# Optimization experiments

Measured on AMD Instinct MI355X. Metric: run time of the kernel, lower is better.

Reference implementation:

```python
import jax, jax.numpy as jnp
import numpy as np

D_MODEL = 1024
H = 16
D_K = D_MODEL // H
D_FF = 4096
EPS = 1e-6
NEG = -1e9


def setup_inputs() -> dict:
    key = jax.random.key(0)
    ks = jax.random.split(key, 8)
    B, S = 2, 2048
    src = jax.random.normal(ks[0], (B, S, D_MODEL), dtype=jnp.float32)
    src_mask = jnp.ones((B, 1, 1, S), dtype=jnp.int32)
    sc = 1.0 / np.sqrt(D_MODEL)
    wq = jax.random.normal(ks[1], (D_MODEL, D_MODEL), jnp.float32) * sc
    wk = jax.random.normal(ks[2], (D_MODEL, D_MODEL), jnp.float32) * sc
    wv = jax.random.normal(ks[3], (D_MODEL, D_MODEL), jnp.float32) * sc
    wo = jax.random.normal(ks[4], (D_MODEL, D_MODEL), jnp.float32) * sc
    w1 = jax.random.normal(ks[5], (D_FF, D_MODEL), jnp.float32) * sc
    b1 = jnp.zeros((D_FF,), jnp.float32)
    w2 = jax.random.normal(ks[6], (D_MODEL, D_FF), jnp.float32) * (1.0 / np.sqrt(D_FF))
    b2 = jnp.zeros((D_MODEL,), jnp.float32)
    a1 = jnp.ones((1,), jnp.float32)
    be1 = jnp.zeros((1,), jnp.float32)
    a2 = jnp.ones((1,), jnp.float32)
    be2 = jnp.zeros((1,), jnp.float32)
    return dict(src=src, src_mask=src_mask, wq=wq, wk=wk, wv=wv, wo=wo,
                w1=w1, b1=b1, w2=w2, b2=b2, a1=a1, be1=be1, a2=a2, be2=be2)


def layer_norm(x, alpha, bias):
    # torch: mean + unbiased std (ddof=1), eps added to std
    mean = jnp.mean(x, axis=-1, keepdims=True)
    std = jnp.sqrt(jnp.var(x, axis=-1, keepdims=True, ddof=1))
    return alpha * (x - mean) / (std + EPS) + bias


def mha(x, mask, wq, wk, wv, wo):
    B, S, _ = x.shape
    def split(t):  # [B,S,D] -> [B,H,S,D_K]
        return t.reshape(B, S, H, D_K).transpose(0, 2, 1, 3)
    q = split(x @ wq.T)
    k = split(x @ wk.T)
    v = split(x @ wv.T)
    scores = jnp.einsum('bhqd,bhkd->bhqk', q, k) / np.sqrt(D_K)
    scores = jnp.where(mask == 0, NEG, scores)
    attn = jax.nn.softmax(scores, axis=-1)
    out = jnp.einsum('bhqk,bhkd->bhqd', attn, v)
    out = out.transpose(0, 2, 1, 3).reshape(B, S, D_MODEL)
    return out @ wo.T


def reference(src, src_mask, wq, wk, wv, wo, w1, b1, w2, b2, a1, be1, a2, be2):
    x = layer_norm(src, a1, be1)
    src = src + mha(x, src_mask, wq, wk, wv, wo)
    x = layer_norm(src, a2, be2)
    ff = jax.nn.relu(x @ w1.T + b1) @ w2.T + b2
    return src + ff
```

## Files before the change

kernel.cpp:

```cpp
#include <hip/hip_runtime.h>
#include <hip/hip_bf16.h>

typedef unsigned short u16;
typedef unsigned int u32;
typedef float floatx4 __attribute__((ext_vector_type(4)));
typedef __bf16 bf16x8 __attribute__((ext_vector_type(8)));
typedef u16 ushort4v __attribute__((ext_vector_type(4)));
typedef u16 ushort8v __attribute__((ext_vector_type(8)));

#define DEVI static __device__ __forceinline__

DEVI u16 f2bf(float f) {
    u32 u = __builtin_bit_cast(u32, f);
    u += 0x7fffu + ((u >> 16) & 1u);
    return (u16)(u >> 16);
}
DEVI float bf2f(u16 h) { return __builtin_bit_cast(float, (u32)h << 16); }

DEVI float fexp2(float x) { return __builtin_amdgcn_exp2f(x); }

DEVI u32 cvtpk_bf16(float lo, float hi) {
    u32 r;
    asm("v_cvt_pk_bf16_f32 %0, %1, %2" : "=v"(r) : "v"(lo), "v"(hi));
    return r;
}

DEVI void async_cp16(const u16* g, u16* l) {
    __builtin_amdgcn_global_load_lds((const __attribute__((address_space(1))) u32*)g,
                                     (__attribute__((address_space(3))) u32*)l, 16, 0, 0);
}

template<int N> DEVI void wait_vmcnt() {
    if constexpr (N == 2)      asm volatile("s_waitcnt vmcnt(2)" ::: "memory");
    else if constexpr (N == 3) asm volatile("s_waitcnt vmcnt(3)" ::: "memory");
    else if constexpr (N == 4) asm volatile("s_waitcnt vmcnt(4)" ::: "memory");
    else if constexpr (N == 6) asm volatile("s_waitcnt vmcnt(6)" ::: "memory");
    else if constexpr (N == 8) asm volatile("s_waitcnt vmcnt(8)" ::: "memory");
    else static_assert(N == 2, "add vmcnt case");
}

template<int BM, int BN, int RW, int CW, bool QKV3, int NSPLIT, bool XSWZ,
         bool BIAS, bool RELU, bool RESID, bool OBF16, bool VTW>
__global__ __launch_bounds__(256) void gemm_nt(
    const u16* __restrict__ A,
    const u16* __restrict__ W0, const u16* __restrict__ W1, const u16* __restrict__ W2,
    const float* __restrict__ bias, const float* __restrict__ resid,
    void* __restrict__ o0, void* __restrict__ o1, void* __restrict__ o2,
    void* __restrict__ o3, int K, int lda, int Nper, int NX)
{
    static_assert(RW * CW == 4, "4 waves");
    constexpr int WM = BM / RW, WN = BN / CW;
    constexpr int MI = WM / 16, NI = WN / 16;
    constexpr int LPT = BM / 64 + BN / 64;
    __shared__ __align__(16) u16 As[3][BM * 32];
    __shared__ __align__(16) u16 Bs[3][BN * 32];
    const int tid = threadIdx.x;
    const int w = tid >> 6, lane = tid & 63;
    const int q = lane >> 4, ml = lane & 15;
    const int wr = w / CW, wc = w % CW;
    int bx = blockIdx.x, by = blockIdx.y;
    if (XSWZ) {
        const int gx = gridDim.x, gy = gridDim.y;
        int L = by * gx + bx;
        int xcd = L & 7, s = L >> 3;
        int mb = gy >> 3;
        by = xcd * mb + s % mb;
        bx = s / mb;
    }
    const int m0 = by * BM;
    size_t kbase = 0;
    const u16* W = W0;
    void* outp = o0;
    if (NSPLIT > 1) {
        int part = bx / NX; bx -= part * NX; kbase = (size_t)part * K;
        outp = (part == 0) ? o0 : (part == 1 ? o1 : (part == 2 ? o2 : o3));
    }
    int n0 = bx * BN;
    bool vwrite = false;
    if (QKV3) {
        int sel = n0 / Nper;
        n0 -= sel * Nper;
        W = (sel == 0) ? W0 : (sel == 1 ? W1 : W2);
        outp = (sel == 0) ? o0 : (sel == 1 ? o1 : o2);
        if (VTW) vwrite = (sel == 2);
    }

    auto stage = [&](int buf, int kt) {
#pragma unroll
        for (int p = 0; p < BM / 64; ++p) {
            int g = p * 256 + tid;
            int r = g >> 2, s = g & 3;
            int c = s ^ ((r >> 1) & 3);
            async_cp16(A + (size_t)(m0 + r) * lda + kbase + kt + c * 8,
                       &As[buf][(p * 256 + w * 64) * 8]);
        }
#pragma unroll
        for (int p = 0; p < BN / 64; ++p) {
            int g = p * 256 + tid;
            int r = g >> 2, s = g & 3;
            int c = s ^ ((r >> 1) & 3);
            async_cp16(W + (size_t)(n0 + r) * lda + kbase + kt + c * 8,
                       &Bs[buf][(p * 256 + w * 64) * 8]);
        }
    };

    const floatx4 fzero = {0.f, 0.f, 0.f, 0.f};
    floatx4 acc[MI][NI];
#pragma unroll
    for (int i = 0; i < MI; ++i)
#pragma unroll
        for (int j = 0; j < NI; ++j) acc[i][j] = fzero;

    const int nt = K >> 5;
    stage(0, 0);
    stage(1, 32);
    int cb = 0, nb = 2;
    for (int it = 0, kt = 0; it < nt; ++it, kt += 32) {
        wait_vmcnt<LPT>();
        __builtin_amdgcn_s_barrier();
        __builtin_amdgcn_sched_barrier(0);
        if (it + 2 < nt) stage(nb, kt + 64);
        __builtin_amdgcn_sched_barrier(0);
        const u16* Asb = As[cb];
        const u16* Bsb = Bs[cb];
        bf16x8 af[MI], bfr[NI];
#pragma unroll
        for (int i = 0; i < MI; ++i) {
            int rm = wr * WM + i * 16 + ml;
            int s = q ^ ((rm >> 1) & 3);
            af[i] = *(const bf16x8*)&Asb[(rm * 4 + s) * 8];
        }
#pragma unroll
        for (int j = 0; j < NI; ++j) {
            int rn = wc * WN + j * 16 + ml;
            int s = q ^ ((rn >> 1) & 3);
            bfr[j] = *(const bf16x8*)&Bsb[(rn * 4 + s) * 8];
        }
#pragma unroll
        for (int i = 0; i < MI; ++i)
#pragma unroll
            for (int j = 0; j < NI; ++j)
                acc[i][j] = __builtin_amdgcn_mfma_f32_16x16x32_bf16(af[i], bfr[j], acc[i][j], 0, 0, 0);
        cb = cb == 2 ? 0 : cb + 1;
        nb = nb == 2 ? 0 : nb + 1;
    }

#pragma unroll
    for (int j = 0; j < NI; ++j) {
        int gn = n0 + wc * WN + j * 16 + ml;
        float bj = 0.f;
        if (BIAS) bj = bias[gn];
#pragma unroll
        for (int i = 0; i < MI; ++i) {
            int gm0 = m0 + wr * WM + i * 16 + q * 4;
            if (VTW && vwrite) {
                int bb = gm0 >> 11, sres = gm0 & 2047;
                ushort4v o = {f2bf(acc[i][j][0]), f2bf(acc[i][j][1]),
                              f2bf(acc[i][j][2]), f2bf(acc[i][j][3])};
                *(ushort4v*)&((u16*)o3)[(size_t)(bb * 1024 + gn) * 2048 + sres] = o;
            } else {
#pragma unroll
                for (int r = 0; r < 4; ++r) {
                    size_t idx = (size_t)(gm0 + r) * Nper + gn;
                    float v = acc[i][j][r] + bj;
                    if (RELU) v = fmaxf(v, 0.f);
                    if (RESID) v += resid[idx];
                    if (OBF16) ((u16*)outp)[idx] = f2bf(v);
                    else       ((float*)outp)[idx] = v;
                }
            }
        }
    }
}

__global__ __launch_bounds__(256, 2) void flash9(
    const u16* __restrict__ Q, const u16* __restrict__ Kg,
    const u16* __restrict__ Vt, const float* __restrict__ biasv,
    u16* __restrict__ O)
{
    __shared__ __align__(16) u16 smem[24576];
    const int tid = threadIdx.x;
    const int w = tid >> 6, lane = tid & 63;
    const int qw = w & 1, kv = w >> 1;
    const int q = lane >> 4, ml = lane & 15;
    const int b = blockIdx.y >> 4, h = blockIdx.y & 15;
    const size_t rowQ = (size_t)(b * 2048 + blockIdx.x * 128);
    const float KSC = 0.125f * 1.4426950408889634f;
    const floatx4 fzero = {0.f, 0.f, 0.f, 0.f};

    bf16x8 qa[4][2];
#pragma unroll
    for (int qg = 0; qg < 4; ++qg)
#pragma unroll
        for (int c = 0; c < 2; ++c)
            qa[qg][c] = *(const bf16x8*)&Q[(rowQ + qw * 64 + qg * 16 + ml) * 1024
                                           + h * 64 + q * 8 + c * 32];

    auto stage = [&](int buf, int it) {
        {
            int row = tid >> 3, sl = tid & 7;
            int ch = sl ^ ((row & 3) | (((row >> 3) & 1) << 2));
#pragma unroll
            for (int hf = 0; hf < 2; ++hf)
                async_cp16(Kg + (size_t)(b * 2048 + hf * 1024 + it * 32 + row) * 1024
                               + h * 64 + ch * 8,
                           &smem[(hf * 3 + buf) * 2048 + w * 512]);
        }
        {
            int row = tid >> 2, sl = tid & 3;
            int ch = sl ^ ((row >> 1) & 3);
#pragma unroll
            for (int hf = 0; hf < 2; ++hf)
                async_cp16(Vt + (size_t)(b * 1024 + h * 64 + row) * 2048
                               + hf * 1024 + it * 32 + ch * 8,
                           &smem[12288 + (hf * 3 + buf) * 2048 + w * 512]);
        }
    };

    floatx4 oacc[4][4];
    float lsum[4] = {0.f, 0.f, 0.f, 0.f};
#pragma unroll
    for (int qg = 0; qg < 4; ++qg)
#pragma unroll
        for (int d = 0; d < 4; ++d) oacc[qg][d] = fzero;

    const int swk = (ml & 3) | (((ml >> 2) & 1) << 2);
    const int re = ((ml >> 2) << 3) + (ml & 3);

    stage(0, 0);
    stage(1, 1);
    int cb = 0, nb = 2;
    for (int it = 0; it < 32; ++it) {
        asm volatile("s_waitcnt vmcnt(4)" ::: "memory");
        __builtin_amdgcn_s_barrier();
        __builtin_amdgcn_sched_barrier(0);
        const int s0 = kv * 1024 + it * 32;
        const float4 be = *(const float4*)&biasv[b * 2048 + s0 + q * 8];
        const float4 bo = *(const float4*)&biasv[b * 2048 + s0 + q * 8 + 4];
        __builtin_amdgcn_sched_barrier(0);
        stage(nb, it + 2 < 32 ? it + 2 : 31);

        const u16* Kb = &smem[(kv * 3 + cb) * 2048];
        const u16* Vb = &smem[12288 + (kv * 3 + cb) * 2048];

        bf16x8 ke0 = *(const bf16x8*)&Kb[(re + 0) * 64 + ((0 + q) ^ swk) * 8];
        bf16x8 ke1 = *(const bf16x8*)&Kb[(re + 0) * 64 + ((4 + q) ^ swk) * 8];
        bf16x8 ko0 = *(const bf16x8*)&Kb[(re + 4) * 64 + ((0 + q) ^ swk) * 8];
        bf16x8 ko1 = *(const bf16x8*)&Kb[(re + 4) * 64 + ((4 + q) ^ swk) * 8];
        bf16x8 pfrag[4];
#pragma unroll
        for (int qg = 0; qg < 4; ++qg) {
            floatx4 te = fzero, to = fzero;
            te = __builtin_amdgcn_mfma_f32_16x16x32_bf16(ke0, qa[qg][0], te, 0, 0, 0);
            te = __builtin_amdgcn_mfma_f32_16x16x32_bf16(ke1, qa[qg][1], te, 0, 0, 0);
            to = __builtin_amdgcn_mfma_f32_16x16x32_bf16(ko0, qa[qg][0], to, 0, 0, 0);
            to = __builtin_amdgcn_mfma_f32_16x16x32_bf16(ko1, qa[qg][1], to, 0, 0, 0);
            float pe0 = fexp2(fmaf(te[0], KSC, be.x));
            float pe1 = fexp2(fmaf(te[1], KSC, be.y));
            float pe2 = fexp2(fmaf(te[2], KSC, be.z));
            float pe3 = fexp2(fmaf(te[3], KSC, be.w));
            float po0 = fexp2(fmaf(to[0], KSC, bo.x));
            float po1 = fexp2(fmaf(to[1], KSC, bo.y));
            float po2 = fexp2(fmaf(to[2], KSC, bo.z));
            float po3 = fexp2(fmaf(to[3], KSC, bo.w));
            lsum[qg] += ((pe0 + pe1) + (pe2 + pe3)) + ((po0 + po1) + (po2 + po3));
            u32 pk[4];
            pk[0] = cvtpk_bf16(pe0, pe1);
            pk[1] = cvtpk_bf16(pe2, pe3);
            pk[2] = cvtpk_bf16(po0, po1);
            pk[3] = cvtpk_bf16(po2, po3);
            pfrag[qg] = __builtin_bit_cast(bf16x8, *(uint4*)pk);
        }
#pragma unroll
        for (int dt = 0; dt < 4; ++dt) {
            int vrow = dt * 16 + ml;
            bf16x8 vf = *(const bf16x8*)&Vb[vrow * 32 + ((q ^ ((vrow >> 1) & 3)) * 8)];
#pragma unroll
            for (int qg = 0; qg < 4; ++qg)
                oacc[qg][dt] = __builtin_amdgcn_mfma_f32_16x16x32_bf16(
                    vf, pfrag[qg], oacc[qg][dt], 0, 0, 0);
        }
        cb = cb == 2 ? 0 : cb + 1;
        nb = nb == 2 ? 0 : nb + 1;
    }

    __syncthreads();
    float* sO = (float*)smem;
    float* sL = (float*)smem + 8192;
    if (kv == 1) {
#pragma unroll
        for (int qg = 0; qg < 4; ++qg) {
            sL[(qw * 4 + qg) * 64 + lane] = lsum[qg];
#pragma unroll
            for (int dt = 0; dt < 4; ++dt)
                *(floatx4*)&sO[((qw * 4 + qg) * 4 + dt) * 256 + lane * 4] = oacc[qg][dt];
        }
    }
    __syncthreads();
    if (kv == 1) return;
#pragma unroll
    for (int qg = 0; qg < 4; ++qg) {
        lsum[qg] += sL[(qw * 4 + qg) * 64 + lane];
#pragma unroll
        for (int dt = 0; dt < 4; ++dt)
            oacc[qg][dt] += *(const floatx4*)&sO[((qw * 4 + qg) * 4 + dt) * 256 + lane * 4];
        float ls = lsum[qg];
        ls += __shfl_xor(ls, 16, 64);
        ls += __shfl_xor(ls, 32, 64);
        const float rcp = 1.f / ls;
        const size_t row = rowQ + qw * 64 + qg * 16 + ml;
#pragma unroll
        for (int dt = 0; dt < 4; ++dt)
#pragma unroll
            for (int rp = 0; rp < 4; rp += 2) {
                u32 pk = (u32)f2bf(oacc[qg][dt][rp] * rcp)
                       | ((u32)f2bf(oacc[qg][dt][rp + 1] * rcp) << 16);
                *(u32*)&O[row * 1024 + h * 64 + dt * 16 + q * 4 + rp] = pk;
            }
    }
}

DEVI void ln_row(const float* __restrict__ x, float ga, float gb,
                 u16* __restrict__ y, int row, int tid)
{
    const float4 v = ((const float4*)(x + (size_t)row * 1024))[tid];
    float s = v.x + v.y + v.z + v.w;
    float ss = v.x * v.x + v.y * v.y + v.z * v.z + v.w * v.w;
#pragma unroll
    for (int d = 1; d < 64; d <<= 1) { s += __shfl_xor(s, d, 64); ss += __shfl_xor(ss, d, 64); }
    __shared__ float ps[4], pss[4];
    const int w = tid >> 6, lane = tid & 63;
    if (lane == 0) { ps[w] = s; pss[w] = ss; }
    __syncthreads();
    s = ps[0] + ps[1] + ps[2] + ps[3];
    ss = pss[0] + pss[1] + pss[2] + pss[3];
    float mean = s * (1.f / 1024.f);
    float var = fmaxf((ss - s * mean) * (1.f / 1023.f), 0.f);
    float sc = ga / (sqrtf(var) + 1e-6f);
    ushort4v o;
    o[0] = f2bf((v.x - mean) * sc + gb);
    o[1] = f2bf((v.y - mean) * sc + gb);
    o[2] = f2bf((v.z - mean) * sc + gb);
    o[3] = f2bf((v.w - mean) * sc + gb);
    ((ushort4v*)(y + (size_t)row * 1024))[tid] = o;
}

__global__ __launch_bounds__(256) void ln_bf16(const float* __restrict__ x,
    const float* __restrict__ ga, const float* __restrict__ gb, u16* __restrict__ y)
{
    ln_row(x, ga[0], gb[0], y, blockIdx.x, threadIdx.x);
}

__global__ __launch_bounds__(256) void prep(
    const float* __restrict__ wq, const float* __restrict__ wk,
    const float* __restrict__ wv, const float* __restrict__ wo,
    const float* __restrict__ w1, const float* __restrict__ w2,
    u16* __restrict__ wqb, u16* __restrict__ wkb, u16* __restrict__ wvb,
    u16* __restrict__ wob, u16* __restrict__ w1b, u16* __restrict__ w2b,
    const int* __restrict__ m, float* __restrict__ biasv,
    const float* __restrict__ src, const float* __restrict__ a1,
    const float* __restrict__ be1, u16* __restrict__ xln1)
{
    const int bx = blockIdx.x;
    if (bx < 12288) {
        size_t i = (size_t)bx * 256 + threadIdx.x;
        const float* s; u16* d; size_t off;
        if (i < 262144)       { s = wq; d = wqb; off = i; }
        else if (i < 524288)  { s = wk; d = wkb; off = i - 262144; }
        else if (i < 786432)  { s = wv; d = wvb; off = i - 524288; }
        else if (i < 1048576) { s = wo; d = wob; off = i - 786432; }
        else if (i < 2097152) { s = w1; d = w1b; off = i - 1048576; }
        else                  { s = w2; d = w2b; off = i - 2097152; }
        float4 v = ((const float4*)s)[off];
        ushort4v o = {f2bf(v.x), f2bf(v.y), f2bf(v.z), f2bf(v.w)};
        ((ushort4v*)d)[off] = o;
    } else if (bx < 12304) {
        int i = (bx - 12288) * 256 + threadIdx.x;
        biasv[i] = m[i] ? 0.f : -1.442695e9f;
    } else {
        ln_row(src, a1[0], be1[0], xln1, bx - 12304, threadIdx.x);
    }
}

__global__ __launch_bounds__(256) void ff2_fin(
    const u16* __restrict__ p0, const u16* __restrict__ p1,
    const float* __restrict__ b2, const float* __restrict__ resid,
    float* __restrict__ out)
{
    const size_t i = (size_t)blockIdx.x * 256 + threadIdx.x;
    ushort4v a = *(const ushort4v*)&p0[i * 4];
    ushort4v b = *(const ushort4v*)&p1[i * 4];
    float4 r = ((const float4*)resid)[i];
    float4 bb = ((const float4*)b2)[i & 255];
    float4 o;
    o.x = (bf2f(a[0]) + bf2f(b[0])) + r.x + bb.x;
    o.y = (bf2f(a[1]) + bf2f(b[1])) + r.y + bb.y;
    o.z = (bf2f(a[2]) + bf2f(b[2])) + r.z + bb.z;
    o.w = (bf2f(a[3]) + bf2f(b[3])) + r.w + bb.w;
    ((float4*)out)[i] = o;
}

extern "C" void kernel_launch(void* const* d_in, const int* in_sizes, int n_in,
                              void* d_out, int out_size, void* d_ws, size_t ws_size,
                              hipStream_t stream)
{
    const float* src = (const float*)d_in[0];
    const int* msk   = (const int*)d_in[1];
    const float* wq  = (const float*)d_in[2];
    const float* wk  = (const float*)d_in[3];
    const float* wv  = (const float*)d_in[4];
    const float* wo  = (const float*)d_in[5];
    const float* w1  = (const float*)d_in[6];
    const float* b1  = (const float*)d_in[7];
    const float* w2  = (const float*)d_in[8];
    const float* b2  = (const float*)d_in[9];
    const float* a1  = (const float*)d_in[10];
    const float* be1 = (const float*)d_in[11];
    const float* a2  = (const float*)d_in[12];
    const float* be2 = (const float*)d_in[13];
    float* out = (float*)d_out;

    char* ws = (char*)d_ws;
    const size_t MB = (size_t)1 << 20;
    u16* wqb  = (u16*)(ws + 0 * MB);
    u16* wkb  = (u16*)(ws + 2 * MB);
    u16* wvb  = (u16*)(ws + 4 * MB);
    u16* wob  = (u16*)(ws + 6 * MB);
    u16* w1b  = (u16*)(ws + 8 * MB);
    u16* w2b  = (u16*)(ws + 16 * MB);
    u16* xln1 = (u16*)(ws + 24 * MB);
    u16* attn = xln1;
    u16* Qb   = (u16*)(ws + 32 * MB);
    u16* xln2 = Qb;
    u16* Kb   = (u16*)(ws + 40 * MB);
    u16* Vt   = (u16*)(ws + 56 * MB);
    float* biasv = (float*)(ws + 64 * MB);
    u16* h1   = (u16*)(ws + 40 * MB);
    float* src2 = (float*)(ws + 72 * MB);
    u16* P0 = (u16*)(ws + 0 * MB);
    u16* P1 = (u16*)(ws + 24 * MB);

    prep<<<16400, 256, 0, stream>>>(wq, wk, wv, wo, w1, w2,
                                    wqb, wkb, wvb, wob, w1b, w2b,
                                    msk, biasv, src, a1, be1, xln1);

    gemm_nt<128, 128, 2, 2, true, 1, true, false, false, false, true, true><<<dim3(24, 32), 256, 0, stream>>>(
        xln1, wqb, wkb, wvb, nullptr, nullptr, Qb, Kb, nullptr, Vt, 1024, 1024, 1024, 0);

    flash9<<<dim3(16, 32), 256, 0, stream>>>(Qb, Kb, Vt, biasv, attn);

    gemm_nt<128, 64, 4, 1, false, 1, true, false, false, true, false, false><<<dim3(16, 32), 256, 0, stream>>>(
        attn, wob, nullptr, nullptr, nullptr, src, src2, nullptr, nullptr, nullptr,
        1024, 1024, 1024, 0);

    ln_bf16<<<4096, 256, 0, stream>>>(src2, a2, be2, xln2);

    gemm_nt<128, 128, 2, 2, false, 1, true, true, true, false, true, false><<<dim3(32, 32), 256, 0, stream>>>(
        xln2, w1b, nullptr, nullptr, b1, nullptr, h1, nullptr, nullptr, nullptr,
        1024, 1024, 4096, 0);

    gemm_nt<128, 128, 2, 2, false, 2, true, false, false, false, true, false><<<dim3(16, 32), 256, 0, stream>>>(
        h1, w2b, nullptr, nullptr, nullptr, nullptr, P0, P1, nullptr, nullptr,
        2048, 4096, 1024, 8);

    ff2_fin<<<4096, 256, 0, stream>>>(P0, P1, b2, src2, out);
}
```

Measured before the change: 334.1 us.

## Add 256x256 8-wave ping-pong GEMM for QKV and FFN, split FF2 K four ways

```diff
diff --git a/kernel.cpp b/kernel.cpp
--- a/kernel.cpp
+++ b/kernel.cpp
@@ -31,22 +31,167 @@
 }
 
 template<int N> DEVI void wait_vmcnt() {
-    if constexpr (N == 2)      asm volatile("s_waitcnt vmcnt(2)" ::: "memory");
+    if constexpr (N == 0)      asm volatile("s_waitcnt vmcnt(0)" ::: "memory");
+    else if constexpr (N == 2) asm volatile("s_waitcnt vmcnt(2)" ::: "memory");
     else if constexpr (N == 3) asm volatile("s_waitcnt vmcnt(3)" ::: "memory");
     else if constexpr (N == 4) asm volatile("s_waitcnt vmcnt(4)" ::: "memory");
     else if constexpr (N == 6) asm volatile("s_waitcnt vmcnt(6)" ::: "memory");
-    else if constexpr (N == 8) asm volatile("s_waitcnt vmcnt(8)" ::: "memory");
-    else static_assert(N == 2, "add vmcnt case");
-}
-
-template<int BM, int BN, int RW, int CW, bool QKV3, int NSPLIT, bool XSWZ,
-         bool BIAS, bool RELU, bool RESID, bool OBF16, bool VTW>
-__global__ __launch_bounds__(256) void gemm_nt(
+    else static_assert(N == 0, "add vmcnt case");
+}
+
+#define PH_BAR() asm volatile("s_barrier" ::: "memory")
+
+template<bool QKV3, int NSPLIT, bool BIAS, bool RELU, bool VTW>
+__global__ __launch_bounds__(512, 2) void gemm8p(
     const u16* __restrict__ A,
     const u16* __restrict__ W0, const u16* __restrict__ W1, const u16* __restrict__ W2,
-    const float* __restrict__ bias, const float* __restrict__ resid,
+    const float* __restrict__ bias,
     void* __restrict__ o0, void* __restrict__ o1, void* __restrict__ o2,
     void* __restrict__ o3, int K, int lda, int Nper, int NX)
+{
+    __shared__ __align__(16) u16 As[2][2][8192];
+    __shared__ __align__(16) u16 Bs[2][2][8192];
+    const int tid = threadIdx.x;
+    const int w = tid >> 6, lane = tid & 63;
+    const int q = lane >> 4, ml = lane & 15;
+    const int wr = w >> 2, wc = w & 3;
+    int bx = blockIdx.x, by = blockIdx.y;
+    {
+        const int gx = gridDim.x, gy = gridDim.y;
+        int L = by * gx + bx;
+        int xcd = L & 7, s = L >> 3;
+        int mb = gy >> 3;
+        by = xcd * mb + s % mb;
+        bx = s / mb;
+    }
+    const int m0 = by * 256;
+    size_t kbase = 0;
+    const u16* W = W0;
+    void* outp = o0;
+    if (NSPLIT > 1) {
+        int part = bx / NX; bx -= part * NX; kbase = (size_t)part * K;
+        outp = (part == 0) ? o0 : (part == 1 ? o1 : (part == 2 ? o2 : o3));
+    }
+    int n0 = bx * 256;
+    bool vwrite = false;
+    if (QKV3) {
+        int sel = n0 / Nper; n0 -= sel * Nper;
+        W = (sel == 0) ? W0 : (sel == 1 ? W1 : W2);
+        outp = (sel == 0) ? o0 : (sel == 1 ? o1 : o2);
+        if (VTW) vwrite = (sel == 2);
+    }
+
+    auto stA = [&](int d, int kh, int kt) {
+#pragma unroll
+        for (int p = 0; p < 2; ++p) {
+            int c = p * 512 + tid;
+            int r = c >> 2;
+            int sc = (c & 3) ^ ((r >> 1) & 3);
+            async_cp16(A + (size_t)(m0 + r) * lda + kbase + kt + kh * 32 + sc * 8,
+                       &As[d][kh][(p * 512 + w * 64) * 8]);
+        }
+    };
+    auto stB = [&](int d, int kh, int kt) {
+#pragma unroll
+        for (int p = 0; p < 2; ++p) {
+            int c = p * 512 + tid;
+            int r = c >> 2;
+            int sc = (c & 3) ^ ((r >> 1) & 3);
+            async_cp16(W + (size_t)(n0 + r) * lda + kbase + kt + kh * 32 + sc * 8,
+                       &Bs[d][kh][(p * 512 + w * 64) * 8]);
+        }
+    };
+    auto rdA = [&](int d, int kh, int i) -> bf16x8 {
+        int rm = wr * 128 + i * 16 + ml;
+        return *(const bf16x8*)&As[d][kh][(rm * 4 + (q ^ ((rm >> 1) & 3))) * 8];
+    };
+    auto rdB = [&](int d, int kh, int j) -> bf16x8 {
+        int rn = wc * 64 + j * 16 + ml;
+        return *(const bf16x8*)&Bs[d][kh][(rn * 4 + (q ^ ((rn >> 1) & 3))) * 8];
+    };
+
+    const floatx4 fzero = {0.f, 0.f, 0.f, 0.f};
+    floatx4 acc[8][4];
+#pragma unroll
+    for (int i = 0; i < 8; ++i)
+#pragma unroll
+        for (int j = 0; j < 4; ++j) acc[i][j] = fzero;
+
+#define PHASE(d, kh, ih, STG, VM)                                              \
+    {                                                                          \
+        if (ih == 0) {                                                         \
+            _Pragma("unroll")                                                  \
+            for (int j = 0; j < 4; ++j) bfr[j] = rdB(d, kh, j);                \
+        }                                                                      \
+        _Pragma("unroll")                                                      \
+        for (int ii = 0; ii < 4; ++ii) af[ii] = rdA(d, kh, (ih) * 4 + ii);     \
+        STG;                                                                   \
+        if (VM) wait_vmcnt<4>();                                               \
+        PH_BAR();                                                              \
+        __builtin_amdgcn_s_setprio(1);                                         \
+        _Pragma("unroll")                                                      \
+        for (int ii = 0; ii < 4; ++ii)                                         \
+            _Pragma("unroll")                                                  \
+            for (int j = 0; j < 4; ++j)                                        \
+                acc[(ih) * 4 + ii][j] = __builtin_amdgcn_mfma_f32_16x16x32_bf16( \
+                    af[ii], bfr[j], acc[(ih) * 4 + ii][j], 0, 0, 0);           \
+        __builtin_amdgcn_s_setprio(0);                                         \
+        PH_BAR();                                                              \
+    }
+
+    const int R = K >> 7;
+    stA(0, 0, 0); stB(0, 0, 0); stA(0, 1, 0); stB(0, 1, 0);
+    wait_vmcnt<0>();
+    PH_BAR();
+
+    for (int rr = 0; rr < R; ++rr) {
+        const int kt1 = rr * 128 + 64;
+        const int kt2 = (rr * 128 + 128 <= K - 64) ? rr * 128 + 128
+                                                   : K - 64;
+        bf16x8 af[4], bfr[4];
+        PHASE(0, 0, 0, stA(1, 0, kt1), 0)
+        PHASE(0, 0, 1, stB(1, 0, kt1), 1)
+        PHASE(0, 1, 0, stA(1, 1, kt1), 0)
+        PHASE(0, 1, 1, stB(1, 1, kt1), 1)
+        PHASE(1, 0, 0, stA(0, 0, kt2), 0)
+        PHASE(1, 0, 1, stB(0, 0, kt2), 1)
+        PHASE(1, 1, 0, stA(0, 1, kt2), 0)
+        PHASE(1, 1, 1, stB(0, 1, kt2), 1)
+    }
+#undef PHASE
+    wait_vmcnt<0>();
+
+#pragma unroll
+    for (int j = 0; j < 4; ++j) {
+        int gn = n0 + wc * 64 + j * 16 + ml;
+        float bj = 0.f;
+        if (BIAS) bj = bias[gn];
+#pragma unroll
+        for (int i = 0; i < 8; ++i) {
+            int gm0 = m0 + wr * 128 + i * 16 + q * 4;
+            if (VTW && vwrite) {
+                int bb = gm0 >> 11, sres = gm0 & 2047;
+                ushort4v o = {f2bf(acc[i][j][0]), f2bf(acc[i][j][1]),
+                              f2bf(acc[i][j][2]), f2bf(acc[i][j][3])};
+                *(ushort4v*)&((u16*)o3)[(size_t)(bb * 1024 + gn) * 2048 + sres] = o;
+            } else {
+#pragma unroll
+                for (int r = 0; r < 4; ++r) {
+                    size_t idx = (size_t)(gm0 + r) * Nper + gn;
+                    float v = acc[i][j][r] + bj;
+                    if (RELU) v = fmaxf(v, 0.f);
+                    ((u16*)outp)[idx] = f2bf(v);
+                }
+            }
+        }
+    }
+}
+
+template<int BM, int BN, int RW, int CW, bool BIAS, bool RELU, bool RESID, bool OBF16>
+__global__ __launch_bounds__(256) void gemm_nt(
+    const u16* __restrict__ A, const u16* __restrict__ W0,
+    const float* __restrict__ bias, const float* __restrict__ resid,
+    void* __restrict__ o0, int K, int lda, int Nper)
 {
     static_assert(RW * CW == 4, "4 waves");
     constexpr int WM = BM / RW, WN = BN / CW;
@@ -59,7 +204,7 @@
     const int q = lane >> 4, ml = lane & 15;
     const int wr = w / CW, wc = w % CW;
     int bx = blockIdx.x, by = blockIdx.y;
-    if (XSWZ) {
+    {
         const int gx = gridDim.x, gy = gridDim.y;
         int L = by * gx + bx;
         int xcd = L & 7, s = L >> 3;
@@ -68,22 +213,8 @@
         bx = s / mb;
     }
     const int m0 = by * BM;
-    size_t kbase = 0;
     const u16* W = W0;
-    void* outp = o0;
-    if (NSPLIT > 1) {
-        int part = bx / NX; bx -= part * NX; kbase = (size_t)part * K;
-        outp = (part == 0) ? o0 : (part == 1 ? o1 : (part == 2 ? o2 : o3));
-    }
     int n0 = bx * BN;
-    bool vwrite = false;
-    if (QKV3) {
-        int sel = n0 / Nper;
-        n0 -= sel * Nper;
-        W = (sel == 0) ? W0 : (sel == 1 ? W1 : W2);
-        outp = (sel == 0) ? o0 : (sel == 1 ? o1 : o2);
-        if (VTW) vwrite = (sel == 2);
-    }
 
     auto stage = [&](int buf, int kt) {
 #pragma unroll
@@ -91,7 +222,7 @@
             int g = p * 256 + tid;
             int r = g >> 2, s = g & 3;
             int c = s ^ ((r >> 1) & 3);
-            async_cp16(A + (size_t)(m0 + r) * lda + kbase + kt + c * 8,
+            async_cp16(A + (size_t)(m0 + r) * lda + kt + c * 8,
                        &As[buf][(p * 256 + w * 64) * 8]);
         }
 #pragma unroll
@@ -99,7 +230,7 @@
             int g = p * 256 + tid;
             int r = g >> 2, s = g & 3;
             int c = s ^ ((r >> 1) & 3);
-            async_cp16(W + (size_t)(n0 + r) * lda + kbase + kt + c * 8,
+            async_cp16(W + (size_t)(n0 + r) * lda + kt + c * 8,
                        &Bs[buf][(p * 256 + w * 64) * 8]);
         }
     };
@@ -153,21 +284,14 @@
 #pragma unroll
         for (int i = 0; i < MI; ++i) {
             int gm0 = m0 + wr * WM + i * 16 + q * 4;
-            if (VTW && vwrite) {
-                int bb = gm0 >> 11, sres = gm0 & 2047;
-                ushort4v o = {f2bf(acc[i][j][0]), f2bf(acc[i][j][1]),
-                              f2bf(acc[i][j][2]), f2bf(acc[i][j][3])};
-                *(ushort4v*)&((u16*)o3)[(size_t)(bb * 1024 + gn) * 2048 + sres] = o;
-            } else {
-#pragma unroll
-                for (int r = 0; r < 4; ++r) {
-                    size_t idx = (size_t)(gm0 + r) * Nper + gn;
-                    float v = acc[i][j][r] + bj;
-                    if (RELU) v = fmaxf(v, 0.f);
-                    if (RESID) v += resid[idx];
-                    if (OBF16) ((u16*)outp)[idx] = f2bf(v);
-                    else       ((float*)outp)[idx] = v;
-                }
+#pragma unroll
+            for (int r = 0; r < 4; ++r) {
+                size_t idx = (size_t)(gm0 + r) * Nper + gn;
+                float v = acc[i][j][r] + bj;
+                if (RELU) v = fmaxf(v, 0.f);
+                if (RESID) v += resid[idx];
+                if (OBF16) ((u16*)o0)[idx] = f2bf(v);
+                else       ((float*)o0)[idx] = v;
             }
         }
     }
@@ -384,19 +508,22 @@
 
 __global__ __launch_bounds__(256) void ff2_fin(
     const u16* __restrict__ p0, const u16* __restrict__ p1,
+    const u16* __restrict__ p2, const u16* __restrict__ p3,
     const float* __restrict__ b2, const float* __restrict__ resid,
     float* __restrict__ out)
 {
     const size_t i = (size_t)blockIdx.x * 256 + threadIdx.x;
     ushort4v a = *(const ushort4v*)&p0[i * 4];
     ushort4v b = *(const ushort4v*)&p1[i * 4];
+    ushort4v c = *(const ushort4v*)&p2[i * 4];
+    ushort4v d = *(const ushort4v*)&p3[i * 4];
     float4 r = ((const float4*)resid)[i];
     float4 bb = ((const float4*)b2)[i & 255];
     float4 o;
-    o.x = (bf2f(a[0]) + bf2f(b[0])) + r.x + bb.x;
-    o.y = (bf2f(a[1]) + bf2f(b[1])) + r.y + bb.y;
-    o.z = (bf2f(a[2]) + bf2f(b[2])) + r.z + bb.z;
-    o.w = (bf2f(a[3]) + bf2f(b[3])) + r.w + bb.w;
+    o.x = ((bf2f(a[0]) + bf2f(b[0])) + (bf2f(c[0]) + bf2f(d[0]))) + r.x + bb.x;
+    o.y = ((bf2f(a[1]) + bf2f(b[1])) + (bf2f(c[1]) + bf2f(d[1]))) + r.y + bb.y;
+    o.z = ((bf2f(a[2]) + bf2f(b[2])) + (bf2f(c[2]) + bf2f(d[2]))) + r.z + bb.z;
+    o.w = ((bf2f(a[3]) + bf2f(b[3])) + (bf2f(c[3]) + bf2f(d[3]))) + r.w + bb.w;
     ((float4*)out)[i] = o;
 }
 
@@ -438,30 +565,31 @@
     u16* h1   = (u16*)(ws + 40 * MB);
     float* src2 = (float*)(ws + 72 * MB);
     u16* P0 = (u16*)(ws + 0 * MB);
-    u16* P1 = (u16*)(ws + 24 * MB);
+    u16* P1 = (u16*)(ws + 8 * MB);
+    u16* P2 = (u16*)(ws + 24 * MB);
+    u16* P3 = (u16*)(ws + 32 * MB);
 
     prep<<<16400, 256, 0, stream>>>(wq, wk, wv, wo, w1, w2,
                                     wqb, wkb, wvb, wob, w1b, w2b,
                                     msk, biasv, src, a1, be1, xln1);
 
-    gemm_nt<128, 128, 2, 2, true, 1, true, false, false, false, true, true><<<dim3(24, 32), 256, 0, stream>>>(
-        xln1, wqb, wkb, wvb, nullptr, nullptr, Qb, Kb, nullptr, Vt, 1024, 1024, 1024, 0);
+    gemm8p<true, 1, false, false, true><<<dim3(12, 16), 512, 0, stream>>>(
+        xln1, wqb, wkb, wvb, nullptr, Qb, Kb, nullptr, Vt, 1024, 1024, 1024, 0);
 
     flash9<<<dim3(16, 32), 256, 0, stream>>>(Qb, Kb, Vt, biasv, attn);
 
-    gemm_nt<128, 64, 4, 1, false, 1, true, false, false, true, false, false><<<dim3(16, 32), 256, 0, stream>>>(
-        attn, wob, nullptr, nullptr, nullptr, src, src2, nullptr, nullptr, nullptr,
-        1024, 1024, 1024, 0);
+    gemm_nt<128, 64, 4, 1, false, false, true, false><<<dim3(16, 32), 256, 0, stream>>>(
+        attn, wob, nullptr, src, src2, 1024, 1024, 1024);
 
     ln_bf16<<<4096, 256, 0, stream>>>(src2, a2, be2, xln2);
 
-    gemm_nt<128, 128, 2, 2, false, 1, true, true, true, false, true, false><<<dim3(32, 32), 256, 0, stream>>>(
-        xln2, w1b, nullptr, nullptr, b1, nullptr, h1, nullptr, nullptr, nullptr,
+    gemm8p<false, 1, true, true, false><<<dim3(16, 16), 512, 0, stream>>>(
+        xln2, w1b, nullptr, nullptr, b1, h1, nullptr, nullptr, nullptr,
         1024, 1024, 4096, 0);
 
-    gemm_nt<128, 128, 2, 2, false, 2, true, false, false, false, true, false><<<dim3(16, 32), 256, 0, stream>>>(
-        h1, w2b, nullptr, nullptr, nullptr, nullptr, P0, P1, nullptr, nullptr,
-        2048, 4096, 1024, 8);
-
-    ff2_fin<<<4096, 256, 0, stream>>>(P0, P1, b2, src2, out);
-}
+    gemm8p<false, 4, false, false, false><<<dim3(16, 16), 512, 0, stream>>>(
+        h1, w2b, nullptr, nullptr, nullptr, P0, P1, P2, P3,
+        1024, 4096, 1024, 4);
+
+    ff2_fin<<<4096, 256, 0, stream>>>(P0, P1, P2, P3, b2, src2, out);
+}
```

Measured after the change: 348.2 us. 1.04x slower.
